# Optimization experiments

Hardware: AMD Instinct MI355X
Metric: run time of the kernel (lower is better)

Reference implementation:

```python
import jax, jax.numpy as jnp
import numpy as np

M = 23          # number of dendritic subunits
N_SYN = 1500    # number of synapses
T = 30000       # timesteps
B = 101         # temporal kernel length (odd -> 'same' output length)
G_NO = 4        # synapse groups (first half excitatory double-exp kernel)
PAD = B // 2
# parent (1-based) of each subunit; 0 marks root; children have higher index
C_DEN = np.array([0] + [((m - 1) // 2) + 1 for m in range(1, M)], dtype=np.int64)
G_ASSIGN = np.arange(N_SYN, dtype=np.int64) % G_NO   # synapse -> group
SYN_SUB = np.arange(N_SYN, dtype=np.int64) % M       # synapse -> subunit (C_syn nonzeros)


def setup_inputs() -> dict:
    key = jax.random.key(0)
    X = jax.random.uniform(key, (T, N_SYN), dtype=jnp.float32)
    V_o = jnp.ones((1,), jnp.float32) * -69.0
    Tau = jnp.ones((G_NO,), jnp.float32) * 1.4
    Delta = jnp.ones((1,), jnp.float32) * 0.25
    W = jnp.concatenate([jnp.full((G_NO // 2,), 2.0, jnp.float32),
                         jnp.full((G_NO - G_NO // 2,), -1.0, jnp.float32)]) * 0.05
    C = jnp.ones((M,), jnp.float32)
    Theta = jnp.zeros((M,), jnp.float32)
    return {"X": X, "V_o": V_o, "Tau": Tau, "Delta": Delta, "W": W, "C": C, "Theta": Theta}


def _group_kernels(Tau, Delta):
    # shared shifted time base, clamped at 0
    t = jnp.maximum(jnp.arange(B, dtype=jnp.float32) - jnp.exp(Delta[0]), 0.0)  # [B]
    tau = jnp.exp(Tau)[:, None]                               # [G_NO, 1]
    tf = t[None, :] / tau
    fast = tf * jnp.exp(-tf)                                   # alpha kernel
    ts = t[None, :] / (tau * 2.8 + 10.4)
    slow = ts * jnp.exp(-ts) * 0.3
    exc = (fast + slow) / 1.3                                  # dual-exp for excitatory groups
    is_exc = (jnp.arange(G_NO) < G_NO // 2)[:, None]
    return jnp.where(is_exc, exc, fast)                        # [G_NO, B]


def _forward(X, V_o, Tau, Delta, W, C, Theta):
    kern = _group_kernels(Tau, Delta)                          # [G_NO, B]
    g = jnp.asarray(G_ASSIGN)
    # conv is linear, so fold the per-group weight W[g] into the kernel
    k_syn = kern[g] * W[g][:, None]                            # [N_SYN, B]
    # depthwise cross-correlation (matches torch F.conv1d), 'same' padding
    filt = jax.lax.conv_general_dilated(
        X.T[None],                 # [1, N, T]
        k_syn[:, None, :],         # [N, 1, B]
        window_strides=(1,), padding=[(PAD, PAD)],
        feature_group_count=N_SYN,
        dimension_numbers=('NCH', 'OIH', 'NCH'))[0].T          # [T, N]
    # gather-sum of synapses into subunits (C_syn sign only selects membership)
    A = jax.nn.one_hot(jnp.asarray(SYN_SUB), M, dtype=X.dtype)  # [N, M]
    sub_in = filt @ A                                           # [T, M]
    expC = jnp.exp(C)
    # internal nodes processed from leaves toward root (descending indices)
    roots = (np.flip(np.unique(C_DEN))[:-1] - 1).astype(int)
    root_set = set(roots.tolist())
    out = [None] * M
    for m in range(M):                                          # leaves
        if m not in root_set:
            out[m] = jax.nn.sigmoid(sub_in[:, m] - Theta[m]) * expC[m]
    for r in roots:                                             # tree reduction
        s = sub_in[:, r]
        for k in np.where(C_DEN == r + 1)[0]:
            s = s + out[k]
        out[r] = jax.nn.sigmoid(s - Theta[r]) * expC[r]
    return out[0] + V_o[0]                                      # [T]


def reference(X, V_o, Tau, Delta, W, C, Theta):
    return _forward(X, V_o, Tau, Delta, W, C, Theta)
```

## Files before the change

kernel.cpp:

```cpp
#include <hip/hip_runtime.h>
#include <cstddef>

#define T_DIM 30000
#define M_DIM 23
#define NJ    92
#define TILE  64
#define STR   184
#define SUBS  25
#define RROWS 8
#define XP4   377
#define WPS   144

typedef short bf16x8 __attribute__((ext_vector_type(8)));
typedef float f32x4  __attribute__((ext_vector_type(4)));

__device__ __forceinline__ unsigned short f2bf(float f) {
    unsigned int u = __float_as_uint(f);
    return (unsigned short)((u + 0x7fffu + ((u >> 16) & 1u)) >> 16);
}

__global__ __launch_bounds__(256) void reduce_k(const float* __restrict__ X,
                                                unsigned short* __restrict__ Yb) {
    __shared__ __align__(16) float4 Xs[RROWS * XP4];

    const int tid = threadIdx.x;
    const int tb  = blockIdx.x * RROWS;

    const float4* Xg = reinterpret_cast<const float4*>(X) + (size_t)tb * 375;
    #pragma unroll
    for (int it = 0; it < 12; ++it) {
        int i = tid + 256 * it;
        if (i < 3000) {
            int r = i / 375;
            int pos = i - r * 375;
            Xs[r * XP4 + pos] = Xg[i];
        }
    }
    __syncthreads();

    if (tid < 184) {
        int r = tid / 23;
        int q = tid - 23 * r;
        const float4* row = &Xs[r * XP4];
        float4 s = make_float4(0.f, 0.f, 0.f, 0.f);
        #pragma unroll
        for (int k = 0; k < 16; ++k) {
            float4 v = row[q + 23 * k];
            s.x += v.x; s.y += v.y; s.z += v.z; s.w += v.w;
        }
        if (q < 7) {
            float4 v = row[q + 23 * 16];
            s.x += v.x; s.y += v.y; s.z += v.z; s.w += v.w;
        }
        ushort4 o;
        o.x = f2bf(s.x); o.y = f2bf(s.y); o.z = f2bf(s.z); o.w = f2bf(s.w);
        reinterpret_cast<ushort4*>(Yb)[(size_t)(tb + r) * 23 + q] = o;
    }
}

__global__ __launch_bounds__(512, 2) void conv_tree_k(
    const unsigned short* __restrict__ Yb,
    const float* __restrict__ Tau,
    const float* __restrict__ Delta,
    const float* __restrict__ W,
    const float* __restrict__ Vo,
    const float* __restrict__ C,
    const float* __restrict__ Theta,
    float* __restrict__ out)
{
    __shared__ __align__(16) unsigned short Yt[NJ * STR];
    __shared__ __align__(16) float wpadT[4 * WPS];
    __shared__ float sub[TILE * SUBS];
    __shared__ float sTheta[M_DIM];
    __shared__ float sExpC[M_DIM];

    const int tid = threadIdx.x;
    const int t0  = blockIdx.x * TILE;
    const int l   = tid & 63;

    {
        float eD = __expf(Delta[0]);
        for (int i = tid; i < 4 * WPS; i += 512) {
            int g = i / WPS;
            int x = (i - g * WPS) - 16;
            float val = 0.f;
            if (x >= 0 && x <= 100) {
                float tt  = fmaxf((float)x - eD, 0.f);
                float tau = __expf(Tau[g]);
                float tf  = tt / tau;
                float fast = tf * __expf(-tf);
                float kv;
                if (g < 2) {
                    float ts = tt / (tau * 2.8f + 10.4f);
                    kv = (fast + ts * __expf(-ts) * 0.3f) * (1.0f / 1.3f);
                } else {
                    kv = fast;
                }
                val = kv * W[g];
            }
            wpadT[i] = val;
        }
    }
    if (tid < M_DIM) {
        sTheta[tid] = Theta[tid];
        sExpC[tid]  = __expf(C[tid]);
    }
    __syncthreads();

    {
        unsigned int* Yw = reinterpret_cast<unsigned int*>(Yt);
        for (int i = tid; i < 88 * 23; i += 512) {
            int rp = i / 23;
            int q  = i - rp * 23;
            int g0 = t0 - 50 + 2 * rp;
            ushort4 ra = make_ushort4(0, 0, 0, 0);
            ushort4 rb = make_ushort4(0, 0, 0, 0);
            if ((unsigned)g0       < (unsigned)T_DIM) ra = reinterpret_cast<const ushort4*>(Yb)[(size_t)g0 * 23 + q];
            if ((unsigned)(g0 + 1) < (unsigned)T_DIM) rb = reinterpret_cast<const ushort4*>(Yb)[(size_t)(g0 + 1) * 23 + q];
            Yw[(q     ) * 92 + rp] = (unsigned)ra.x | ((unsigned)rb.x << 16);
            Yw[(q + 23) * 92 + rp] = (unsigned)ra.y | ((unsigned)rb.y << 16);
            Yw[(q + 46) * 92 + rp] = (unsigned)ra.z | ((unsigned)rb.z << 16);
            Yw[(q + 69) * 92 + rp] = (unsigned)ra.w | ((unsigned)rb.w << 16);
        }
    }

    const int n    = l & 15;
    const int kq   = (l >> 4) << 3;
    uint4 af[16];
    #pragma unroll
    for (int g = 0; g < 4; ++g) {
        const float* wp = &wpadT[g * WPS + 16 - n + kq];
        #pragma unroll
        for (int kk = 0; kk < 4; ++kk) {
            const float* wk8 = wp + kk * 32;
            unsigned int d[4];
            #pragma unroll
            for (int p = 0; p < 4; ++p) {
                unsigned short lo = f2bf(wk8[2 * p]);
                unsigned short hi = f2bf(wk8[2 * p + 1]);
                d[p] = (unsigned)lo | ((unsigned)hi << 16);
            }
            af[g * 4 + kk] = make_uint4(d[0], d[1], d[2], d[3]);
        }
    }

    const int wave = tid >> 6;
    const int dt   = (wave & 3) * 16;
    const int nt   = wave >> 2;
    const int m    = nt * 16 + n;
    const bool mvalid = (m < M_DIM);
    const int mc   = mvalid ? m : 0;

    __syncthreads();

    f32x4 acc = {0.f, 0.f, 0.f, 0.f};
    #pragma unroll
    for (int g = 0; g < 4; ++g) {
        int a  = (3 * ((g - mc) & 3)) & 3;
        int j  = mc + 23 * a;
        int cp = (j >> 2) + 23 * g;
        const unsigned short* colp = &Yt[cp * STR + dt + kq];

        bf16x8 b0 = *reinterpret_cast<const bf16x8*>(colp);
        acc = __builtin_amdgcn_mfma_f32_16x16x32_bf16(__builtin_bit_cast(bf16x8, af[g*4+0]), b0, acc, 0, 0, 0);
        bf16x8 b1 = *reinterpret_cast<const bf16x8*>(colp + 32);
        acc = __builtin_amdgcn_mfma_f32_16x16x32_bf16(__builtin_bit_cast(bf16x8, af[g*4+1]), b1, acc, 0, 0, 0);
        bf16x8 b2 = *reinterpret_cast<const bf16x8*>(colp + 64);
        acc = __builtin_amdgcn_mfma_f32_16x16x32_bf16(__builtin_bit_cast(bf16x8, af[g*4+2]), b2, acc, 0, 0, 0);
        bf16x8 b3 = *reinterpret_cast<const bf16x8*>(colp + 96);
        acc = __builtin_amdgcn_mfma_f32_16x16x32_bf16(__builtin_bit_cast(bf16x8, af[g*4+3]), b3, acc, 0, 0, 0);
    }

    if (mvalid) {
        int i0 = (l >> 4) * 4;
        #pragma unroll
        for (int r = 0; r < 4; ++r)
            sub[(dt + i0 + r) * SUBS + m] = acc[r];
    }
    __syncthreads();

    if (tid < TILE) {
        int t = t0 + tid;
        if (t < T_DIM) {
            const float* s = &sub[tid * SUBS];
            float o[M_DIM];
            #pragma unroll
            for (int mm = 11; mm < 23; ++mm) {
                float x = s[mm] - sTheta[mm];
                o[mm] = sExpC[mm] / (1.f + __expf(-x));
            }
            #pragma unroll
            for (int rr = 10; rr >= 0; --rr) {
                float x = s[rr] + o[2 * rr + 1] + o[2 * rr + 2] - sTheta[rr];
                o[rr] = sExpC[rr] / (1.f + __expf(-x));
            }
            out[t] = o[0] + Vo[0];
        }
    }
}

extern "C" void kernel_launch(void* const* d_in, const int* in_sizes, int n_in,
                              void* d_out, int out_size, void* d_ws, size_t ws_size,
                              hipStream_t stream) {
    const float* X     = (const float*)d_in[0];
    const float* Vo    = (const float*)d_in[1];
    const float* Tau   = (const float*)d_in[2];
    const float* Delta = (const float*)d_in[3];
    const float* W     = (const float*)d_in[4];
    const float* C     = (const float*)d_in[5];
    const float* Theta = (const float*)d_in[6];
    float* out = (float*)d_out;
    unsigned short* Yb = (unsigned short*)d_ws;

    reduce_k<<<T_DIM / RROWS, 256, 0, stream>>>(X, Yb);
    conv_tree_k<<<(T_DIM + TILE - 1) / TILE, 512, 0, stream>>>(
        Yb, Tau, Delta, W, Vo, C, Theta, out);
}
```

Measured before the change: 43.48 us.

## Fuse reduce and conv-tree kernels with a grid-wide atomic barrier

```diff
diff --git a/kernel.cpp b/kernel.cpp
--- a/kernel.cpp
+++ b/kernel.cpp
@@ -7,9 +7,10 @@
 #define TILE  64
 #define STR   184
 #define SUBS  25
-#define RROWS 8
 #define XP4   377
 #define WPS   144
+#define NBLK  469
+#define RGRP  8
 
 typedef short bf16x8 __attribute__((ext_vector_type(8)));
 typedef float f32x4  __attribute__((ext_vector_type(4)));
@@ -19,65 +20,30 @@
     return (unsigned short)((u + 0x7fffu + ((u >> 16) & 1u)) >> 16);
 }
 
-__global__ __launch_bounds__(256) void reduce_k(const float* __restrict__ X,
-                                                unsigned short* __restrict__ Yb) {
-    __shared__ __align__(16) float4 Xs[RROWS * XP4];
-
-    const int tid = threadIdx.x;
-    const int tb  = blockIdx.x * RROWS;
-
-    const float4* Xg = reinterpret_cast<const float4*>(X) + (size_t)tb * 375;
-    #pragma unroll
-    for (int it = 0; it < 12; ++it) {
-        int i = tid + 256 * it;
-        if (i < 3000) {
-            int r = i / 375;
-            int pos = i - r * 375;
-            Xs[r * XP4 + pos] = Xg[i];
-        }
-    }
-    __syncthreads();
-
-    if (tid < 184) {
-        int r = tid / 23;
-        int q = tid - 23 * r;
-        const float4* row = &Xs[r * XP4];
-        float4 s = make_float4(0.f, 0.f, 0.f, 0.f);
-        #pragma unroll
-        for (int k = 0; k < 16; ++k) {
-            float4 v = row[q + 23 * k];
-            s.x += v.x; s.y += v.y; s.z += v.z; s.w += v.w;
-        }
-        if (q < 7) {
-            float4 v = row[q + 23 * 16];
-            s.x += v.x; s.y += v.y; s.z += v.z; s.w += v.w;
-        }
-        ushort4 o;
-        o.x = f2bf(s.x); o.y = f2bf(s.y); o.z = f2bf(s.z); o.w = f2bf(s.w);
-        reinterpret_cast<ushort4*>(Yb)[(size_t)(tb + r) * 23 + q] = o;
-    }
-}
-
-__global__ __launch_bounds__(512, 2) void conv_tree_k(
-    const unsigned short* __restrict__ Yb,
+__global__ __launch_bounds__(512, 4) void fused_k(
+    const float* __restrict__ X,
     const float* __restrict__ Tau,
     const float* __restrict__ Delta,
     const float* __restrict__ W,
     const float* __restrict__ Vo,
     const float* __restrict__ C,
     const float* __restrict__ Theta,
+    unsigned short* __restrict__ Yb,
+    unsigned int* counter,
     float* __restrict__ out)
 {
-    __shared__ __align__(16) unsigned short Yt[NJ * STR];
+    __shared__ __align__(16) unsigned char arena[8 * XP4 * 16];
     __shared__ __align__(16) float wpadT[4 * WPS];
-    __shared__ float sub[TILE * SUBS];
     __shared__ float sTheta[M_DIM];
     __shared__ float sExpC[M_DIM];
 
     const int tid = threadIdx.x;
-    const int t0  = blockIdx.x * TILE;
-    const int l   = tid & 63;
-
+    const int b   = blockIdx.x;
+
+    if (tid < M_DIM) {
+        sTheta[tid] = Theta[tid];
+        sExpC[tid]  = __expf(C[tid]);
+    }
     {
         float eD = __expf(Delta[0]);
         for (int i = tid; i < 4 * WPS; i += 512) {
@@ -101,11 +67,60 @@
             wpadT[i] = val;
         }
     }
-    if (tid < M_DIM) {
-        sTheta[tid] = Theta[tid];
-        sExpC[tid]  = __expf(C[tid]);
+
+    {
+        float4* Xs = reinterpret_cast<float4*>(arena);
+        for (int s = 0; s < RGRP; ++s) {
+            int g8 = b * RGRP + s;
+            if (g8 >= 3750) break;
+            int tb = g8 * 8;
+            const float4* Xg = reinterpret_cast<const float4*>(X) + (size_t)tb * 375;
+            #pragma unroll
+            for (int it = 0; it < 6; ++it) {
+                int i = tid + 512 * it;
+                if (i < 3000) {
+                    int r = i / 375;
+                    int pos = i - r * 375;
+                    Xs[r * XP4 + pos] = Xg[i];
+                }
+            }
+            __syncthreads();
+            if (tid < 184) {
+                int r = tid / 23;
+                int q = tid - 23 * r;
+                const float4* row = &Xs[r * XP4];
+                float4 sm = make_float4(0.f, 0.f, 0.f, 0.f);
+                #pragma unroll
+                for (int k = 0; k < 16; ++k) {
+                    float4 v = row[q + 23 * k];
+                    sm.x += v.x; sm.y += v.y; sm.z += v.z; sm.w += v.w;
+                }
+                if (q < 7) {
+                    float4 v = row[q + 23 * 16];
+                    sm.x += v.x; sm.y += v.y; sm.z += v.z; sm.w += v.w;
+                }
+                ushort4 o;
+                o.x = f2bf(sm.x); o.y = f2bf(sm.y); o.z = f2bf(sm.z); o.w = f2bf(sm.w);
+                reinterpret_cast<ushort4*>(Yb)[(size_t)(tb + r) * 23 + q] = o;
+            }
+            __syncthreads();
+        }
+    }
+
+    if (tid == 0) {
+        __threadfence();
+        atomicAdd(counter, 1u);
+        while (atomicAdd(counter, 0u) < NBLK)
+            __builtin_amdgcn_s_sleep(2);
+        __threadfence();
     }
     __syncthreads();
+
+    unsigned short* Yt = reinterpret_cast<unsigned short*>(arena);
+    float* sub = reinterpret_cast<float*>(arena + NJ * STR * 2);
+
+    const int t0 = b * TILE;
+    const int l  = tid & 63;
 
     {
         unsigned int* Yw = reinterpret_cast<unsigned int*>(Yt);
@@ -124,8 +139,8 @@
         }
     }
 
-    const int n    = l & 15;
-    const int kq   = (l >> 4) << 3;
+    const int n  = l & 15;
+    const int kq = (l >> 4) << 3;
     uint4 af[16];
     #pragma unroll
     for (int g = 0; g < 4; ++g) {
@@ -210,9 +225,10 @@
     const float* C     = (const float*)d_in[5];
     const float* Theta = (const float*)d_in[6];
     float* out = (float*)d_out;
-    unsigned short* Yb = (unsigned short*)d_ws;
-
-    reduce_k<<<T_DIM / RROWS, 256, 0, stream>>>(X, Yb);
-    conv_tree_k<<<(T_DIM + TILE - 1) / TILE, 512, 0, stream>>>(
-        Yb, Tau, Delta, W, Vo, C, Theta, out);
+
+    unsigned short* Yb   = (unsigned short*)d_ws;
+    unsigned int* counter = (unsigned int*)((char*)d_ws + (size_t)T_DIM * NJ * 2);
+
+    hipMemsetAsync(counter, 0, sizeof(unsigned int), stream);
+    fused_k<<<NBLK, 512, 0, stream>>>(X, Tau, Delta, W, Vo, C, Theta, Yb, counter, out);
 }
```

Result: slower. 101.6 us (+133.7%).
